# Kernel optimization log

Measured on AMD Instinct MI355X. Metric: run time of the kernel, lower is better.

The kernel has to match this reference:

```python
import jax, jax.numpy as jnp
import numpy as np

B, S, H = 8, 2048, 1024
NEG = -1e10


def setup_inputs() -> dict:
    key = jax.random.key(0)
    ks = jax.random.split(key, 8)
    scale = 1.0 / np.sqrt(H)
    return {
        "x": jax.random.normal(ks[0], (B, S, H), dtype=jnp.float32),
        "pad_mask": jax.random.randint(ks[1], (B, S), 0, 2, dtype=jnp.int32),
        "Wq": jax.random.uniform(ks[2], (H, H), jnp.float32, -scale, scale),
        "bq": jax.random.uniform(ks[3], (H,), jnp.float32, -scale, scale),
        "Wk": jax.random.uniform(ks[4], (H, H), jnp.float32, -scale, scale),
        "bk": jax.random.uniform(ks[5], (H,), jnp.float32, -scale, scale),
        "Wv": jax.random.uniform(ks[6], (H, H), jnp.float32, -scale, scale),
        "bv": jax.random.uniform(ks[7], (H,), jnp.float32, -scale, scale),
    }


def reference(x, pad_mask, Wq, bq, Wk, bk, Wv, bv):
    # Linear projections (torch Linear: x @ W.T + b)
    q = x @ Wq.T + bq  # [B,S,H]
    k = x @ Wk.T + bk
    v = x @ Wv.T + bv
    weight = jnp.einsum("bid,bjd->bij", q, k)  # [B,S,S]
    seq = x.shape[1]
    # causal mask (strictly upper triangular) + padding mask over key positions
    causal = jnp.triu(jnp.ones((seq, seq), dtype=jnp.float32), k=1)  # [S,S]
    pad = pad_mask.astype(jnp.float32)[:, None, :]  # [B,1,S] -> key axis
    mask = (causal[None, :, :] + pad) > 0  # [B,S,S]
    # torch code fills BEFORE scaling; replicate exactly
    weight = jnp.where(mask, NEG, weight)
    score = jax.nn.softmax(weight / jnp.sqrt(jnp.float32(weight.shape[-1] * 0 + x.shape[-1])), axis=-1)
    return jnp.einsum("bij,bjd->bid", score, v)
```

## Files before the change

### kernel.cpp

```cpp
#include <hip/hip_runtime.h>

typedef __attribute__((ext_vector_type(8))) short short8;
typedef __attribute__((ext_vector_type(4))) short short4v;
typedef __attribute__((ext_vector_type(4))) float float4v;

typedef const __attribute__((address_space(1))) unsigned int* gptr_t;
typedef __attribute__((address_space(3))) unsigned int* lptr_t;

__device__ __forceinline__ unsigned short f2bf(float f) {
  unsigned u = __float_as_uint(f);
  u += 0x7FFFu + ((u >> 16) & 1u);
  return (unsigned short)(u >> 16);
}
__device__ __forceinline__ float bf2f(unsigned short h) {
  return __uint_as_float(((unsigned)h) << 16);
}

__global__ __launch_bounds__(256) void cvt_bf16_kernel(const float* __restrict__ in,
                                                       unsigned short* __restrict__ out,
                                                       int n4) {
  int i = blockIdx.x * 256 + threadIdx.x;
  if (i >= n4) return;
  float4v v = ((const float4v*)in)[i];
  short4v o;
  o[0] = (short)f2bf(v[0]);
  o[1] = (short)f2bf(v[1]);
  o[2] = (short)f2bf(v[2]);
  o[3] = (short)f2bf(v[3]);
  ((short4v*)out)[i] = o;
}

__global__ __launch_bounds__(256) void compact_kernel(const int* __restrict__ pad,
                                                      int* __restrict__ jmap,
                                                      int* __restrict__ cntb,
                                                      float* __restrict__ mean_x) {
  int b = blockIdx.x;
  const int* prow = pad + b * 2048;
  int t = threadIdx.x;
  float4v z = {0.f, 0.f, 0.f, 0.f};
  ((float4v*)(mean_x + b * 1024))[t] = z;
  int base = t * 8;
  int ind[8], incl[8];
  int s = 0;
#pragma unroll
  for (int e = 0; e < 8; ++e) {
    ind[e] = (prow[base + e] == 0);
    s += ind[e];
    incl[e] = s;
  }
  int lane = t & 63, wv = t >> 6;
  int v = s;
#pragma unroll
  for (int off = 1; off < 64; off <<= 1) {
    int u = __shfl_up(v, off);
    if (lane >= off) v += u;
  }
  __shared__ int wsum[4];
  if (lane == 63) wsum[wv] = v;
  __syncthreads();
  int wbase = 0;
  for (int w = 0; w < wv; ++w) wbase += wsum[w];
  int excl_base = wbase + v - s;
#pragma unroll
  for (int e = 0; e < 8; ++e) {
    int cnt_i = excl_base + incl[e];
    cntb[b * 2048 + base + e] = cnt_i;
    if (ind[e]) jmap[b * 2048 + cnt_i - 1] = base + e;
  }
}

__global__ __launch_bounds__(256) void gatherX_kernel(const unsigned short* __restrict__ xb,
                                                      const int* __restrict__ jmap,
                                                      const int* __restrict__ cntb,
                                                      unsigned short* __restrict__ xc) {
  int jc = blockIdx.x, b = blockIdx.y;
  int Nc = cntb[b * 2048 + 2047];
  int W = (Nc + 127) & ~127;
  if (jc >= W) return;
  short4v* dst = (short4v*)(xc + ((size_t)(b * 2048 + jc)) * 1024);
  if (jc < Nc) {
    int j = jmap[b * 2048 + jc];
    const short4v* src = (const short4v*)(xb + ((size_t)(b * 2048 + j)) * 1024);
    dst[threadIdx.x] = src[threadIdx.x];
  } else {
    short4v z = {0, 0, 0, 0};
    dst[threadIdx.x] = z;
  }
}

__global__ __launch_bounds__(256) void meanx_kernel(const unsigned short* __restrict__ xb,
                                                    float* __restrict__ mean_x) {
  int b = blockIdx.x, hblk = blockIdx.y, iblk = blockIdx.z;
  int h = hblk * 256 + threadIdx.x;
  float s = 0.f;
  const unsigned short* base = xb + ((size_t)b * 2048 + (size_t)iblk * 256) * 1024 + h;
  for (int i = 0; i < 256; ++i) s += bf2f(base[(size_t)i * 1024]);
  atomicAdd(&mean_x[b * 1024 + h], s);
}

__global__ __launch_bounds__(256) void gemv_kernel(const float* __restrict__ mean_x,
                                                   const unsigned short* __restrict__ wv,
                                                   const float* __restrict__ bv,
                                                   float* __restrict__ fixmean) {
  int b = blockIdx.x, dblk = blockIdx.y;
  int d = dblk * 256 + threadIdx.x;
  const unsigned short* wrow = wv + (size_t)d * 1024;
  const float* mx = mean_x + b * 1024;
  float s = 0.f;
  for (int h = 0; h < 1024; h += 8) {
    short8 w = *(const short8*)(wrow + h);
#pragma unroll
    for (int e = 0; e < 8; ++e) s += mx[h + e] * bf2f(((const unsigned short*)&w)[e]);
  }
  fixmean[b * 1024 + d] = s * (1.0f / 2048.0f) + bv[d];
}

template <int MODE>
__global__ __launch_bounds__(256, 4) void gemm_bt_kernel(
    const unsigned short* __restrict__ A, const unsigned short* __restrict__ A2,
    const unsigned short* __restrict__ B,
    const float* __restrict__ b1, const float* __restrict__ b2, const float* __restrict__ b3,
    void* __restrict__ C, unsigned short* __restrict__ C2, unsigned short* __restrict__ C3,
    const int* __restrict__ cnt,
    int K, int lda, int ldb, int ldc, size_t sA, size_t sB, size_t sC) {
  int bx = blockIdx.x, by = blockIdx.y, bz = blockIdx.z;
  const unsigned short* Aptr = A;
  if (MODE == 0) {
    int wg = by * 24 + bx;
    int s = (wg & 7) * 384 + (wg >> 3);
    bx = s % 24;
    by = s / 24;
    int r = bx >> 3;
    if (r > 0) {
      int b = by >> 4;
      if (((by & 15) << 7) >= cnt[(b << 11) + 2047]) return;
      Aptr = A2;
    }
  }
  int Kend = K;
  if (MODE == 1) {
    int tc = cnt[(bz << 11) + (by * 128 + 127)];
    if (bx * 128 >= tc) return;
  }
  if (MODE == 2) {
    int tc = cnt[(bz << 11) + (by * 128 + 127)];
    Kend = (tc + 63) & ~63;
  }

  __shared__ __align__(16) char lds[32768];
  char* ldsA = lds;
  char* ldsB = lds + 16384;

  int tid = threadIdx.x;
  int wave = tid >> 6, lane = tid & 63;
  int lm = lane & 15, g = lane >> 4;
  int wm = wave >> 1, wn = wave & 1;
  int swl = (lm & 7) << 4;

  float4v acc[4][4];
#pragma unroll
  for (int i = 0; i < 4; ++i)
#pragma unroll
    for (int j = 0; j < 4; ++j) {
      float4v z = {0.f, 0.f, 0.f, 0.f};
      acc[i][j] = z;
    }

  const char* Abase = (const char*)(Aptr + sA * (size_t)bz + (size_t)(by * 128) * (size_t)lda);
  const char* Bbase = (const char*)(B + sB * (size_t)bz + (size_t)(bx * 128) * (size_t)ldb);
  size_t strideA = (size_t)lda * 2u;
  size_t strideB = (size_t)ldb * 2u;

  int Lbase = wave * 1024 + lane * 16;

  for (int kt = 0; kt < Kend; kt += 64) {
#pragma unroll
    for (int c = 0; c < 4; ++c) {
      int L = c * 4096 + Lbase;
      int row = L >> 7;
      int lb = (L & 127) ^ ((row & 7) << 4);
      const char* ga = Abase + (size_t)row * strideA + (size_t)(kt * 2) + lb;
      __builtin_amdgcn_global_load_lds((gptr_t)(const void*)ga,
                                       (lptr_t)(void*)(ldsA + c * 4096 + wave * 1024), 16, 0, 0);
      const char* gb = Bbase + (size_t)row * strideB + (size_t)(kt * 2) + lb;
      __builtin_amdgcn_global_load_lds((gptr_t)(const void*)gb,
                                       (lptr_t)(void*)(ldsB + c * 4096 + wave * 1024), 16, 0, 0);
    }
    __syncthreads();

#pragma unroll
    for (int k0 = 0; k0 < 64; k0 += 32) {
      short8 af[4], bfv[4];
      int b0 = (k0 * 2 + 16 * g) ^ swl;
#pragma unroll
      for (int mi = 0; mi < 4; ++mi) {
        const char* p = ldsA + (wm * 64 + mi * 16 + lm) * 128;
        af[mi] = *(const short8*)(p + b0);
      }
#pragma unroll
      for (int ni = 0; ni < 4; ++ni) {
        const char* p = ldsB + (wn * 64 + ni * 16 + lm) * 128;
        bfv[ni] = *(const short8*)(p + b0);
      }
#pragma unroll
      for (int mi = 0; mi < 4; ++mi)
#pragma unroll
        for (int ni = 0; ni < 4; ++ni)
          acc[mi][ni] =
              __builtin_amdgcn_mfma_f32_16x16x32_bf16(af[mi], bfv[ni], acc[mi][ni], 0, 0, 0);
    }
    __syncthreads();
  }

  int mb = by * 128 + wm * 64 + g * 4;
  int nb = bx * 128 + wn * 64 + lm;
#pragma unroll
  for (int mi = 0; mi < 4; ++mi) {
#pragma unroll
    for (int ni = 0; ni < 4; ++ni) {
      int n = nb + ni * 16;
      float bias = 0.0f;
      if (MODE == 0) {
        int nn = n & 1023;
        int r = n >> 10;
        bias = (r == 0) ? b1[nn] : ((r == 1) ? b2[nn] : b3[nn]);
      }
#pragma unroll
      for (int r4 = 0; r4 < 4; ++r4) {
        int m = mb + mi * 16 + r4;
        float v = acc[mi][ni][r4] + bias;
        if (MODE == 0) {
          int nn = n & 1023;
          int r = n >> 10;
          if (r == 0) {
            ((unsigned short*)C)[(size_t)m * 1024u + nn] = f2bf(v);
          } else if (r == 1) {
            C3[(size_t)m * 1024u + nn] = f2bf(v);
          } else {
            size_t idx = ((size_t)(m >> 11) << 21) + ((size_t)nn << 11) + (size_t)(m & 2047);
            C2[idx] = f2bf(v);
          }
        } else if (MODE == 1) {
          ((unsigned short*)C)[sC * (size_t)bz + (size_t)m * (size_t)ldc + n] = f2bf(v);
        } else {
          ((float*)C)[sC * (size_t)bz + (size_t)m * (size_t)ldc + n] = v;
        }
      }
    }
  }
}

__global__ __launch_bounds__(256) void softmax_kernel(unsigned short* __restrict__ sp,
                                                      const int* __restrict__ cntb) {
  int i = blockIdx.x, b = blockIdx.y;
  int cnt_i = cntb[b * 2048 + i];
  int tcnt = cntb[b * 2048 + (i | 127)];
  int W = (tcnt + 127) & ~127;
  unsigned short* row = sp + ((size_t)b * 2048 + (size_t)i) * 2048;
  int tid = threadIdx.x;
  int j0 = tid * 8;
  bool active = (j0 < W);

  float t[8];
  if (active) {
    short8 sv = *(const short8*)(row + j0);
#pragma unroll
    for (int e = 0; e < 8; ++e) {
      int jc = j0 + e;
      bool msk = (jc >= cnt_i);
      float raw = bf2f(((const unsigned short*)&sv)[e]);
      t[e] = (msk ? -1e10f : raw) * 0.03125f;
    }
  } else {
#pragma unroll
    for (int e = 0; e < 8; ++e) t[e] = -1e10f * 0.03125f;
  }

  float m = t[0];
#pragma unroll
  for (int e = 1; e < 8; ++e) m = fmaxf(m, t[e]);
#pragma unroll
  for (int o = 32; o > 0; o >>= 1) m = fmaxf(m, __shfl_xor(m, o));
  __shared__ float redm[4], reds[4];
  int wv = tid >> 6, ln = tid & 63;
  if (ln == 0) redm[wv] = m;
  __syncthreads();
  m = fmaxf(fmaxf(redm[0], redm[1]), fmaxf(redm[2], redm[3]));

  float p[8];
  float s = 0.f;
#pragma unroll
  for (int e = 0; e < 8; ++e) {
    p[e] = __expf(t[e] - m);
    s += p[e];
  }
#pragma unroll
  for (int o = 32; o > 0; o >>= 1) s += __shfl_xor(s, o);
  if (ln == 0) reds[wv] = s;
  __syncthreads();
  s = reds[0] + reds[1] + reds[2] + reds[3];
  float inv = 1.0f / s;

  if (active) {
    short8 ov;
#pragma unroll
    for (int e = 0; e < 8; ++e) ((unsigned short*)&ov)[e] = (short)f2bf(p[e] * inv);
    *(short8*)(row + j0) = ov;
  }
}

__global__ __launch_bounds__(256) void fixup_apply_kernel(const int* __restrict__ cntb,
                                                          const float* __restrict__ fixmean,
                                                          float* __restrict__ out) {
  int b = blockIdx.x, dchunk = blockIdx.y;
  int d = dchunk * 256 + threadIdx.x;
  float val = fixmean[b * 1024 + d];
  for (int i = 0; i < 2048; ++i) {
    if (cntb[b * 2048 + i] != 0) break;
    out[((size_t)b * 2048 + (size_t)i) * 1024 + d] = val;
  }
}

extern "C" void kernel_launch(void* const* d_in, const int* in_sizes, int n_in,
                              void* d_out, int out_size, void* d_ws, size_t ws_size,
                              hipStream_t stream) {
  const float* x = (const float*)d_in[0];
  const int* pad = (const int*)d_in[1];
  const float* Wq = (const float*)d_in[2];
  const float* bq = (const float*)d_in[3];
  const float* Wk = (const float*)d_in[4];
  const float* bk = (const float*)d_in[5];
  const float* Wv = (const float*)d_in[6];
  const float* bv = (const float*)d_in[7];
  float* out = (float*)d_out;

  char* ws = (char*)d_ws;
  unsigned short* xb  = (unsigned short*)(ws + 0);
  unsigned short* kc  = (unsigned short*)(ws + 0);
  unsigned short* xc  = (unsigned short*)(ws + 33554432);
  unsigned short* wb  = (unsigned short*)(ws + 67108864);
  int*   jmap    = (int*)(ws + 73400320);
  int*   cntb    = (int*)(ws + 73465856);
  float* mean_x  = (float*)(ws + 73531392);
  float* fixmean = (float*)(ws + 73564160);
  unsigned short* qb  = (unsigned short*)(ws + 75497472);
  unsigned short* vtc = (unsigned short*)(ws + 109051904);
  unsigned short* sp  = (unsigned short*)(ws + 142606336);
  unsigned short* kcb = (unsigned short*)(ws + 209715200);

  cvt_bf16_kernel<<<16384, 256, 0, stream>>>(x, xb, 4194304);
  cvt_bf16_kernel<<<1024, 256, 0, stream>>>(Wq, wb, 262144);
  cvt_bf16_kernel<<<1024, 256, 0, stream>>>(Wk, wb + 1048576, 262144);
  cvt_bf16_kernel<<<1024, 256, 0, stream>>>(Wv, wb + 2097152, 262144);

  compact_kernel<<<8, 256, 0, stream>>>(pad, jmap, cntb, mean_x);
  dim3 gx(2048, 8);
  gatherX_kernel<<<gx, 256, 0, stream>>>(xb, jmap, cntb, xc);
  dim3 gmx(8, 4, 8);
  meanx_kernel<<<gmx, 256, 0, stream>>>(xb, mean_x);

  dim3 g1(24, 128, 1);
  gemm_bt_kernel<0><<<g1, 256, 0, stream>>>(xb, xc, wb, bq, bk, bv, qb, vtc, kcb, cntb,
                                            1024, 1024, 1024, 1024, 0, 0, 0);

  dim3 g3(8, 4);
  gemv_kernel<<<g3, 256, 0, stream>>>(mean_x, wb + 2097152, bv, fixmean);

  dim3 g4(16, 16, 8);
  gemm_bt_kernel<1><<<g4, 256, 0, stream>>>(qb, nullptr, kcb, nullptr, nullptr, nullptr,
                                            sp, nullptr, nullptr, cntb,
                                            1024, 1024, 1024, 2048, 2097152, 2097152, 4194304);

  dim3 g5(2048, 8);
  softmax_kernel<<<g5, 256, 0, stream>>>(sp, cntb);

  dim3 g6(8, 16, 8);
  gemm_bt_kernel<2><<<g6, 256, 0, stream>>>(sp, nullptr, vtc, nullptr, nullptr, nullptr,
                                            out, nullptr, nullptr, cntb,
                                            2048, 2048, 2048, 1024, 4194304, 2097152, 2097152);

  fixup_apply_kernel<<<g3, 256, 0, stream>>>(cntb, fixmean, out);
}
```

Before: 300.7 us.

## Fuse x conversion with compaction gather, merge weight casts, use 128x64 tiles for attention GEMMs

The fp32-to-bf16 conversion of x now also scatters unpadded rows straight into the compacted buffer, so the separate gather pass that re-read xb is dropped. A small kernel zero-fills only the padded tail rows. The three weight conversions are merged into one launch. The QK^T and PV GEMMs switch to 128x64 tiles with 32 rows per wave, giving finer-grained skipping of masked key columns and more workgroups, at the cost of less register-level reuse per tile.

```diff
diff --git a/kernel.cpp b/kernel.cpp
--- a/kernel.cpp
+++ b/kernel.cpp
@@ -16,18 +16,22 @@
   return __uint_as_float(((unsigned)h) << 16);
 }
 
-__global__ __launch_bounds__(256) void cvt_bf16_kernel(const float* __restrict__ in,
-                                                       unsigned short* __restrict__ out,
-                                                       int n4) {
-  int i = blockIdx.x * 256 + threadIdx.x;
-  if (i >= n4) return;
-  float4v v = ((const float4v*)in)[i];
+__global__ __launch_bounds__(256) void cvtW_kernel(const float* __restrict__ Wq,
+                                                   const float* __restrict__ Wk,
+                                                   const float* __restrict__ Wv,
+                                                   unsigned short* __restrict__ wb) {
+  int blk = blockIdx.x;
+  int r = blk >> 10;
+  const float* src = (r == 0) ? Wq : ((r == 1) ? Wk : Wv);
+  int t = threadIdx.x;
+  int i = (blk & 1023) * 256 + t;
+  float4v v = ((const float4v*)src)[i];
   short4v o;
   o[0] = (short)f2bf(v[0]);
   o[1] = (short)f2bf(v[1]);
   o[2] = (short)f2bf(v[2]);
   o[3] = (short)f2bf(v[3]);
-  ((short4v*)out)[i] = o;
+  ((short4v*)(wb + (size_t)r * 1048576u))[i] = o;
 }
 
 __global__ __launch_bounds__(256) void compact_kernel(const int* __restrict__ pad,
@@ -69,23 +73,36 @@
   }
 }
 
-__global__ __launch_bounds__(256) void gatherX_kernel(const unsigned short* __restrict__ xb,
-                                                      const int* __restrict__ jmap,
-                                                      const int* __restrict__ cntb,
-                                                      unsigned short* __restrict__ xc) {
-  int jc = blockIdx.x, b = blockIdx.y;
+__global__ __launch_bounds__(256) void prep_kernel(const float* __restrict__ x,
+                                                   const int* __restrict__ pad,
+                                                   const int* __restrict__ cntb,
+                                                   unsigned short* __restrict__ xb,
+                                                   unsigned short* __restrict__ xc) {
+  int i = blockIdx.x, b = blockIdx.y;
+  int idx = b * 2048 + i;
+  int t = threadIdx.x;
+  float4v v = ((const float4v*)(x + (size_t)idx * 1024))[t];
+  short4v o;
+  o[0] = (short)f2bf(v[0]);
+  o[1] = (short)f2bf(v[1]);
+  o[2] = (short)f2bf(v[2]);
+  o[3] = (short)f2bf(v[3]);
+  ((short4v*)(xb + (size_t)idx * 1024))[t] = o;
+  if (pad[idx] == 0) {
+    int jc = cntb[idx] - 1;
+    ((short4v*)(xc + ((size_t)(b * 2048 + jc)) * 1024))[t] = o;
+  }
+}
+
+__global__ __launch_bounds__(256) void zerofillX_kernel(const int* __restrict__ cntb,
+                                                        unsigned short* __restrict__ xc) {
+  int b = blockIdx.y;
   int Nc = cntb[b * 2048 + 2047];
   int W = (Nc + 127) & ~127;
+  int jc = Nc + blockIdx.x;
   if (jc >= W) return;
-  short4v* dst = (short4v*)(xc + ((size_t)(b * 2048 + jc)) * 1024);
-  if (jc < Nc) {
-    int j = jmap[b * 2048 + jc];
-    const short4v* src = (const short4v*)(xb + ((size_t)(b * 2048 + j)) * 1024);
-    dst[threadIdx.x] = src[threadIdx.x];
-  } else {
-    short4v z = {0, 0, 0, 0};
-    dst[threadIdx.x] = z;
-  }
+  short4v z = {0, 0, 0, 0};
+  ((short4v*)(xc + ((size_t)(b * 2048 + jc)) * 1024))[threadIdx.x] = z;
 }
 
 __global__ __launch_bounds__(256) void meanx_kernel(const unsigned short* __restrict__ xb,
@@ -123,6 +140,10 @@
     void* __restrict__ C, unsigned short* __restrict__ C2, unsigned short* __restrict__ C3,
     const int* __restrict__ cnt,
     int K, int lda, int ldb, int ldc, size_t sA, size_t sB, size_t sC) {
+  constexpr int BN = (MODE == 0) ? 128 : 64;
+  constexpr int BCH = (MODE == 0) ? 4 : 2;
+  constexpr int MI = (MODE == 0) ? 4 : 2;
+
   int bx = blockIdx.x, by = blockIdx.y, bz = blockIdx.z;
   const unsigned short* Aptr = A;
   if (MODE == 0) {
@@ -140,14 +161,14 @@
   int Kend = K;
   if (MODE == 1) {
     int tc = cnt[(bz << 11) + (by * 128 + 127)];
-    if (bx * 128 >= tc) return;
+    if (bx * 64 >= tc) return;
   }
   if (MODE == 2) {
     int tc = cnt[(bz << 11) + (by * 128 + 127)];
     Kend = (tc + 63) & ~63;
   }
 
-  __shared__ __align__(16) char lds[32768];
+  __shared__ __align__(16) char lds[16384 + BN * 128];
   char* ldsA = lds;
   char* ldsB = lds + 16384;
 
@@ -157,9 +178,9 @@
   int wm = wave >> 1, wn = wave & 1;
   int swl = (lm & 7) << 4;
 
-  float4v acc[4][4];
-#pragma unroll
-  for (int i = 0; i < 4; ++i)
+  float4v acc[MI][4];
+#pragma unroll
+  for (int i = 0; i < MI; ++i)
 #pragma unroll
     for (int j = 0; j < 4; ++j) {
       float4v z = {0.f, 0.f, 0.f, 0.f};
@@ -167,7 +188,7 @@
     }
 
   const char* Abase = (const char*)(Aptr + sA * (size_t)bz + (size_t)(by * 128) * (size_t)lda);
-  const char* Bbase = (const char*)(B + sB * (size_t)bz + (size_t)(bx * 128) * (size_t)ldb);
+  const char* Bbase = (const char*)(B + sB * (size_t)bz + (size_t)(bx * BN) * (size_t)ldb);
   size_t strideA = (size_t)lda * 2u;
   size_t strideB = (size_t)ldb * 2u;
 
@@ -182,6 +203,12 @@
       const char* ga = Abase + (size_t)row * strideA + (size_t)(kt * 2) + lb;
       __builtin_amdgcn_global_load_lds((gptr_t)(const void*)ga,
                                        (lptr_t)(void*)(ldsA + c * 4096 + wave * 1024), 16, 0, 0);
+    }
+#pragma unroll
+    for (int c = 0; c < BCH; ++c) {
+      int L = c * 4096 + Lbase;
+      int row = L >> 7;
+      int lb = (L & 127) ^ ((row & 7) << 4);
       const char* gb = Bbase + (size_t)row * strideB + (size_t)(kt * 2) + lb;
       __builtin_amdgcn_global_load_lds((gptr_t)(const void*)gb,
                                        (lptr_t)(void*)(ldsB + c * 4096 + wave * 1024), 16, 0, 0);
@@ -190,20 +217,20 @@
 
 #pragma unroll
     for (int k0 = 0; k0 < 64; k0 += 32) {
-      short8 af[4], bfv[4];
+      short8 af[MI], bfv[4];
       int b0 = (k0 * 2 + 16 * g) ^ swl;
 #pragma unroll
-      for (int mi = 0; mi < 4; ++mi) {
-        const char* p = ldsA + (wm * 64 + mi * 16 + lm) * 128;
-        af[mi] = *(const short8*)(p + b0);
+      for (int mi = 0; mi < MI; ++mi) {
+        int ra = (MODE == 0 ? wm * 64 : wave * 32) + mi * 16 + lm;
+        af[mi] = *(const short8*)(ldsA + ra * 128 + b0);
       }
 #pragma unroll
       for (int ni = 0; ni < 4; ++ni) {
-        const char* p = ldsB + (wn * 64 + ni * 16 + lm) * 128;
-        bfv[ni] = *(const short8*)(p + b0);
+        int rb = (MODE == 0 ? wn * 64 : 0) + ni * 16 + lm;
+        bfv[ni] = *(const short8*)(ldsB + rb * 128 + b0);
       }
 #pragma unroll
-      for (int mi = 0; mi < 4; ++mi)
+      for (int mi = 0; mi < MI; ++mi)
 #pragma unroll
         for (int ni = 0; ni < 4; ++ni)
           acc[mi][ni] =
@@ -212,10 +239,10 @@
     __syncthreads();
   }
 
-  int mb = by * 128 + wm * 64 + g * 4;
-  int nb = bx * 128 + wn * 64 + lm;
-#pragma unroll
-  for (int mi = 0; mi < 4; ++mi) {
+  int mb = by * 128 + (MODE == 0 ? wm * 64 : wave * 32) + g * 4;
+  int nb = bx * BN + (MODE == 0 ? wn * 64 : 0) + lm;
+#pragma unroll
+  for (int mi = 0; mi < MI; ++mi) {
 #pragma unroll
     for (int ni = 0; ni < 4; ++ni) {
       int n = nb + ni * 16;
@@ -255,7 +282,7 @@
   int i = blockIdx.x, b = blockIdx.y;
   int cnt_i = cntb[b * 2048 + i];
   int tcnt = cntb[b * 2048 + (i | 127)];
-  int W = (tcnt + 127) & ~127;
+  int W = (tcnt + 63) & ~63;
   unsigned short* row = sp + ((size_t)b * 2048 + (size_t)i) * 2048;
   int tid = threadIdx.x;
   int j0 = tid * 8;
@@ -336,7 +363,6 @@
 
   char* ws = (char*)d_ws;
   unsigned short* xb  = (unsigned short*)(ws + 0);
-  unsigned short* kc  = (unsigned short*)(ws + 0);
   unsigned short* xc  = (unsigned short*)(ws + 33554432);
   unsigned short* wb  = (unsigned short*)(ws + 67108864);
   int*   jmap    = (int*)(ws + 73400320);
@@ -348,14 +374,13 @@
   unsigned short* sp  = (unsigned short*)(ws + 142606336);
   unsigned short* kcb = (unsigned short*)(ws + 209715200);
 
-  cvt_bf16_kernel<<<16384, 256, 0, stream>>>(x, xb, 4194304);
-  cvt_bf16_kernel<<<1024, 256, 0, stream>>>(Wq, wb, 262144);
-  cvt_bf16_kernel<<<1024, 256, 0, stream>>>(Wk, wb + 1048576, 262144);
-  cvt_bf16_kernel<<<1024, 256, 0, stream>>>(Wv, wb + 2097152, 262144);
-
   compact_kernel<<<8, 256, 0, stream>>>(pad, jmap, cntb, mean_x);
-  dim3 gx(2048, 8);
-  gatherX_kernel<<<gx, 256, 0, stream>>>(xb, jmap, cntb, xc);
+
+  cvtW_kernel<<<3072, 256, 0, stream>>>(Wq, Wk, Wv, wb);
+  dim3 gp(2048, 8);
+  prep_kernel<<<gp, 256, 0, stream>>>(x, pad, cntb, xb, xc);
+  dim3 gz(128, 8);
+  zerofillX_kernel<<<gz, 256, 0, stream>>>(cntb, xc);
   dim3 gmx(8, 4, 8);
   meanx_kernel<<<gmx, 256, 0, stream>>>(xb, mean_x);
 
@@ -366,7 +391,7 @@
   dim3 g3(8, 4);
   gemv_kernel<<<g3, 256, 0, stream>>>(mean_x, wb + 2097152, bv, fixmean);
 
-  dim3 g4(16, 16, 8);
+  dim3 g4(32, 16, 8);
   gemm_bt_kernel<1><<<g4, 256, 0, stream>>>(qb, nullptr, kcb, nullptr, nullptr, nullptr,
                                             sp, nullptr, nullptr, cntb,
                                             1024, 1024, 1024, 2048, 2097152, 2097152, 4194304);
@@ -374,7 +399,7 @@
   dim3 g5(2048, 8);
   softmax_kernel<<<g5, 256, 0, stream>>>(sp, cntb);
 
-  dim3 g6(8, 16, 8);
+  dim3 g6(16, 16, 8);
   gemm_bt_kernel<2><<<g6, 256, 0, stream>>>(sp, nullptr, vtc, nullptr, nullptr, nullptr,
                                             out, nullptr, nullptr, cntb,
                                             2048, 2048, 2048, 1024, 4194304, 2097152, 2097152);
```

After: 308.1 us. 2.5% more time.
